# Kernel optimization log

Measured on AMD Instinct MI355X. Metric: run time of the kernel, lower is better.

## Reference

```python
import jax, jax.numpy as jnp
import numpy as np

TEMPERATURE = 0.5
EPS = 1e-8  # torch.nn.CosineSimilarity default eps


def setup_inputs() -> dict:
    key = jax.random.key(0)
    k1, k2 = jax.random.split(key)
    B, D = 4096, 256
    z1 = jax.random.normal(k1, (B, D), dtype=jnp.float32)
    # z2 = perturbed view of z1 so positive cosine sims are positive
    # (original torch code takes log of the RAW cosine sim, which is NaN
    #  for negative positives; realistic SimCLR positives are correlated views)
    z2 = z1 + 0.1 * jax.random.normal(k2, (B, D), dtype=jnp.float32)
    return {"z1": z1, "z2": z2}


def reference(z1, z2):
    B = z1.shape[0]
    z = jnp.concatenate([z1, z2], axis=0)                      # [2B, D]
    norm = jnp.maximum(jnp.linalg.norm(z, axis=-1, keepdims=True), EPS)
    zn = z / norm
    sim = zn @ zn.T                                            # [2B, 2B] cosine sims
    # positives: sim[i, i+B] and sim[i+B, i] (RAW cosine, per original code)
    pos = jnp.concatenate([jnp.diagonal(sim, offset=B),
                           jnp.diagonal(sim, offset=-B)])      # [2B]
    # mask self-similarity diagonal to -inf before exp-sum
    diag = jnp.eye(2 * B, dtype=bool)
    sim_masked = jnp.where(diag, -jnp.inf, sim)
    denom = jnp.sum(jnp.exp(sim_masked / TEMPERATURE), axis=-1)  # [2B]
    loss = -jnp.mean(jnp.log(pos / denom))
    return loss
```

## Files before the change

### kernel.cpp

```cpp
#include <hip/hip_runtime.h>
#include <hip/hip_bf16.h>


#define NROWS 8192
#define BHALF 4096
#define DDIM  256

typedef __attribute__((ext_vector_type(4))) int   i32x4;
typedef __attribute__((ext_vector_type(8))) int   i32x8;
typedef __attribute__((ext_vector_type(4))) float f32x4;

#define SCALE1 0x7F7F7F7F
#define TWO_LOG2E 2.8853900817779268f

__device__ __forceinline__ void load_lds16(const unsigned char* g, unsigned char* l) {
    __builtin_amdgcn_global_load_lds(
        (const __attribute__((address_space(1))) void*)g,
        (__attribute__((address_space(3))) void*)l, 16, 0, 0);
}

__global__ __launch_bounds__(256) void prep_kernel(const float* __restrict__ z1,
                                                   const float* __restrict__ z2,
                                                   unsigned char* __restrict__ zn8,
                                                   float* __restrict__ posPart,
                                                   float* __restrict__ out) {
    __shared__ float sp[4];
    int wave = threadIdx.x >> 6;
    int lane = threadIdx.x & 63;
    int i    = blockIdx.x * 4 + wave;
    float4 a = reinterpret_cast<const float4*>(z1 + (size_t)i * DDIM)[lane];
    float4 b = reinterpret_cast<const float4*>(z2 + (size_t)i * DDIM)[lane];
    float ss1 = a.x * a.x + a.y * a.y + a.z * a.z + a.w * a.w;
    float ss2 = b.x * b.x + b.y * b.y + b.z * b.z + b.w * b.w;
    float dd  = a.x * b.x + a.y * b.y + a.z * b.z + a.w * b.w;
    #pragma unroll
    for (int off = 32; off; off >>= 1) {
        ss1 += __shfl_xor(ss1, off);
        ss2 += __shfl_xor(ss2, off);
        dd  += __shfl_xor(dd, off);
    }
    float n1 = fmaxf(sqrtf(ss1), 1e-8f);
    float n2 = fmaxf(sqrtf(ss2), 1e-8f);
    float i1 = 1.0f / n1, i2 = 1.0f / n2;
    int pa = __builtin_amdgcn_cvt_pk_fp8_f32(a.x * i1, a.y * i1, 0, 0);
    pa     = __builtin_amdgcn_cvt_pk_fp8_f32(a.z * i1, a.w * i1, pa, 1);
    int pb = __builtin_amdgcn_cvt_pk_fp8_f32(b.x * i2, b.y * i2, 0, 0);
    pb     = __builtin_amdgcn_cvt_pk_fp8_f32(b.z * i2, b.w * i2, pb, 1);
    reinterpret_cast<int*>(zn8 + (size_t)i * DDIM)[lane] = pa;
    reinterpret_cast<int*>(zn8 + (size_t)(i + BHALF) * DDIM)[lane] = pb;
    if (lane == 0) sp[wave] = __logf(dd * i1 * i2);
    if (blockIdx.x == 0 && threadIdx.x == 64) out[0] = 0.0f;
    __syncthreads();
    if (threadIdx.x == 0)
        posPart[blockIdx.x] = sp[0] + sp[1] + sp[2] + sp[3];
}

__global__ __launch_bounds__(256, 3) void denom_kernel(const unsigned char* __restrict__ zn8,
                                                       float* __restrict__ P) {
    __shared__ __align__(16) unsigned char sMem[48 * 1024];
    unsigned char* sA  = sMem;
    unsigned char* sB0 = sMem + 32768;
    unsigned char* sB1 = sMem;
    float* red    = (float*)(sMem + 16384);
    float* colRed = red + 256;

    int x = blockIdx.x, y = blockIdx.y;
    int bi, bj;
    if (x > y) { bi = y;      bj = x - 1;  }
    else       { bi = 63 - y; bj = 63 - x; }
    int iBase = bi * 128;
    int jBase = bj * 128;
    bool isDiag = (bi == bj);

    int t    = threadIdx.x;
    int lane = t & 63;
    int wave = t >> 6;
    int col  = lane & 15;
    int quad = lane >> 4;
    int wm = wave >> 1, wn = wave & 1;

    int rowL  = t >> 4;
    int chunk = (t & 15) ^ rowL;

    {
        const unsigned char* gA = zn8 + (size_t)(iBase + rowL) * DDIM + chunk * 16;
        #pragma unroll
        for (int q = 0; q < 8; q++)
            load_lds16(gA + q * 4096, sA + t * 16 + q * 4096);
        const unsigned char* gB = zn8 + (size_t)(jBase + rowL) * DDIM + chunk * 16;
        #pragma unroll
        for (int q = 0; q < 4; q++)
            load_lds16(gB + q * 4096, sB0 + t * 16 + q * 4096);
    }
    __syncthreads();

    i32x8 af[4][2];
    {
        const unsigned char* aRow = sA + (size_t)(wm * 64 + col) * DDIM;
        #pragma unroll
        for (int mt = 0; mt < 4; mt++)
            #pragma unroll
            for (int ks = 0; ks < 2; ks++) {
                int g0 = ks * 8 + quad * 2;
                i32x4 lo = *(const i32x4*)(aRow + mt * 16 * DDIM + ((g0    ) ^ col) * 16);
                i32x4 hi = *(const i32x4*)(aRow + mt * 16 * DDIM + ((g0 + 1) ^ col) * 16);
                af[mt][ks] = __builtin_shufflevector(lo, hi, 0, 1, 2, 3, 4, 5, 6, 7);
            }
    }
    __syncthreads();

    {
        const unsigned char* gB = zn8 + (size_t)(jBase + 64 + rowL) * DDIM + chunk * 16;
        #pragma unroll
        for (int q = 0; q < 4; q++)
            load_lds16(gB + q * 4096, sB1 + t * 16 + q * 4096);
    }

    float rs[4][4];
    #pragma unroll
    for (int mt = 0; mt < 4; mt++)
        #pragma unroll
        for (int r = 0; r < 4; r++) rs[mt][r] = 0.f;

    #pragma unroll
    for (int h = 0; h < 2; h++) {
        if (h) __syncthreads();
        const unsigned char* bRow =
            (h ? sB1 : sB0) + (size_t)(wn * 32 + col) * DDIM;

        i32x8 bfr[2][2];
        #pragma unroll
        for (int nt = 0; nt < 2; nt++)
            #pragma unroll
            for (int ks = 0; ks < 2; ks++) {
                int g0 = ks * 8 + quad * 2;
                i32x4 lo = *(const i32x4*)(bRow + nt * 16 * DDIM + ((g0    ) ^ col) * 16);
                i32x4 hi = *(const i32x4*)(bRow + nt * 16 * DDIM + ((g0 + 1) ^ col) * 16);
                bfr[nt][ks] = __builtin_shufflevector(lo, hi, 0, 1, 2, 3, 4, 5, 6, 7);
            }

        float cs[2] = {0.f, 0.f};
        #pragma unroll
        for (int mt = 0; mt < 4; mt++) {
            int gi = iBase + wm * 64 + mt * 16;
            #pragma unroll
            for (int nt = 0; nt < 2; nt++) {
                f32x4 acc = {0.f, 0.f, 0.f, 0.f};
                acc = __builtin_amdgcn_mfma_scale_f32_16x16x128_f8f6f4(
                          af[mt][0], bfr[nt][0], acc, 0, 0, 0, SCALE1, 0, SCALE1);
                acc = __builtin_amdgcn_mfma_scale_f32_16x16x128_f8f6f4(
                          af[mt][1], bfr[nt][1], acc, 0, 0, 0, SCALE1, 0, SCALE1);
                bool dtile = (gi == jBase + h * 64 + wn * 32 + nt * 16);
                float csl = 0.f;
                #pragma unroll
                for (int r = 0; r < 4; r++) {
                    float e = exp2f(acc[r] * TWO_LOG2E);
                    if (dtile && (quad * 4 + r) == col) e = 0.f;
                    rs[mt][r] += e;
                    csl += e;
                }
                cs[nt] += csl;
            }
        }

        if (!isDiag) {
            #pragma unroll
            for (int nt = 0; nt < 2; nt++) {
                float v = cs[nt];
                v += __shfl_xor(v, 16);
                v += __shfl_xor(v, 32);
                if (quad == 0)
                    colRed[wm * 128 + h * 64 + wn * 32 + nt * 16 + col] = v;
            }
        }
    }

    #pragma unroll
    for (int mt = 0; mt < 4; mt++)
        #pragma unroll
        for (int r = 0; r < 4; r++) {
            float v = rs[mt][r];
            v += __shfl_xor(v, 1);
            v += __shfl_xor(v, 2);
            v += __shfl_xor(v, 4);
            v += __shfl_xor(v, 8);
            rs[mt][r] = v;
        }
    __syncthreads();
    if (col == 0) {
        #pragma unroll
        for (int mt = 0; mt < 4; mt++)
            #pragma unroll
            for (int r = 0; r < 4; r++)
                red[wn * 128 + wm * 64 + mt * 16 + quad * 4 + r] = rs[mt][r];
    }
    __syncthreads();
    if (t < 128) {
        float* Prow = P + (((size_t)bi * 64 + bj) << 7);
        Prow[t] = red[t] + red[128 + t];
        if (!isDiag) {
            float* Pcol = P + (((size_t)bj * 64 + bi) << 7);
            Pcol[t] = colRed[t] + colRed[128 + t];
        }
    }
}

__global__ __launch_bounds__(256) void loss_kernel(const float* __restrict__ posPart,
                                                   const float* __restrict__ P,
                                                   float* __restrict__ out) {
    __shared__ float sdata[4];
    int t = threadIdx.x;
    int i = blockIdx.x * 256 + t;
    int bi = i >> 7, r = i & 127;
    const float* p = P + ((size_t)bi << 13) + r;
    float d0 = 0.f, d1 = 0.f, d2 = 0.f, d3 = 0.f;
    #pragma unroll
    for (int k = 0; k < 64; k += 4) {
        d0 += p[(k + 0) << 7];
        d1 += p[(k + 1) << 7];
        d2 += p[(k + 2) << 7];
        d3 += p[(k + 3) << 7];
    }
    float s = __logf((d0 + d1) + (d2 + d3));
    if (t < 32) s -= 2.0f * posPart[blockIdx.x * 32 + t];
    #pragma unroll
    for (int off = 32; off; off >>= 1) s += __shfl_xor(s, off);
    if ((t & 63) == 0) sdata[t >> 6] = s;
    __syncthreads();
    if (t == 0)
        atomicAdd(out, (sdata[0] + sdata[1] + sdata[2] + sdata[3]) * (1.0f / NROWS));
}

extern "C" void kernel_launch(void* const* d_in, const int* in_sizes, int n_in,
                              void* d_out, int out_size, void* d_ws, size_t ws_size,
                              hipStream_t stream) {
    const float* z1 = (const float*)d_in[0];
    const float* z2 = (const float*)d_in[1];

    unsigned char* zn8 = (unsigned char*)d_ws;
    float* P       = (float*)((char*)d_ws + (size_t)NROWS * DDIM);
    float* posPart = P + 64 * 64 * 128;

    prep_kernel<<<BHALF / 4, 256, 0, stream>>>(z1, z2, zn8, posPart, (float*)d_out);
    denom_kernel<<<dim3(65, 32), 256, 0, stream>>>(zn8, P);
    loss_kernel<<<NROWS / 256, 256, 0, stream>>>(posPart, P, (float*)d_out);
}
```

Measured before the change: 86.59 us.

## Process four column tiles per block with triple-buffered LDS pipeline

Each denom block now keeps its A row-tile in registers and sweeps up to four consecutive upper-triangular column tiles, streaming B half-tiles through a three-buffer LDS ring with explicit vmcnt waits so loads overlap MFMA/exp work. This cuts the grid from 2080 blocks to 544 and amortises the A load across tiles. Per-wave partial sums are written directly to a doubled P buffer instead of going through LDS reductions, and loss_kernel reads twice as many partials to match. The fixed buffer rotation and per-row tile distribution add complexity and can leave some blocks doing redundant clamped work on the last tile. With fewer blocks there is also less parallelism across CUs.

Result: slower. 105.9 us (+22.3%).

```diff
diff --git a/kernel.cpp b/kernel.cpp
--- a/kernel.cpp
+++ b/kernel.cpp
@@ -58,19 +58,15 @@
 __global__ __launch_bounds__(256, 3) void denom_kernel(const unsigned char* __restrict__ zn8,
                                                        float* __restrict__ P) {
     __shared__ __align__(16) unsigned char sMem[48 * 1024];
-    unsigned char* sA  = sMem;
-    unsigned char* sB0 = sMem + 32768;
-    unsigned char* sB1 = sMem;
-    float* red    = (float*)(sMem + 16384);
-    float* colRed = red + 256;
-
-    int x = blockIdx.x, y = blockIdx.y;
-    int bi, bj;
-    if (x > y) { bi = y;      bj = x - 1;  }
-    else       { bi = 63 - y; bj = 63 - x; }
+    unsigned char* buf0 = sMem;
+    unsigned char* buf1 = sMem + 16384;
+    unsigned char* buf2 = sMem + 32768;
+
+    int b = blockIdx.x;
+    int bi = 0;
+    while (true) { int c = (67 - bi) >> 2; if (b < c) break; b -= c; bi++; }
+    int bjStart = bi + b * 4;
     int iBase = bi * 128;
-    int jBase = bj * 128;
-    bool isDiag = (bi == bj);
 
     int t    = threadIdx.x;
     int lane = t & 63;
@@ -82,21 +78,25 @@
     int rowL  = t >> 4;
     int chunk = (t & 15) ^ rowL;
 
-    {
-        const unsigned char* gA = zn8 + (size_t)(iBase + rowL) * DDIM + chunk * 16;
-        #pragma unroll
-        for (int q = 0; q < 8; q++)
-            load_lds16(gA + q * 4096, sA + t * 16 + q * 4096);
-        const unsigned char* gB = zn8 + (size_t)(jBase + rowL) * DDIM + chunk * 16;
-        #pragma unroll
-        for (int q = 0; q < 4; q++)
-            load_lds16(gB + q * 4096, sB0 + t * 16 + q * 4096);
-    }
-    __syncthreads();
+    unsigned char* bufs[3] = { buf0, buf1, buf2 };
+
+    #define STAGE_HALF(R, DST)                                                  \
+        {                                                                       \
+            const unsigned char* _g = zn8 + (size_t)((R) + rowL) * DDIM + chunk * 16; \
+            _Pragma("unroll")                                                   \
+            for (int q = 0; q < 4; q++)                                         \
+                load_lds16(_g + q * 4096, (DST) + t * 16 + q * 4096);           \
+        }
+
+    STAGE_HALF(iBase,          buf0);
+    STAGE_HALF(iBase + 64,     buf1);
+    STAGE_HALF(bjStart * 128,  buf2);
+    asm volatile("s_waitcnt vmcnt(4)" ::: "memory");
+    __builtin_amdgcn_s_barrier();
 
     i32x8 af[4][2];
     {
-        const unsigned char* aRow = sA + (size_t)(wm * 64 + col) * DDIM;
+        const unsigned char* aRow = (wm ? buf1 : buf0) + (size_t)col * DDIM;
         #pragma unroll
         for (int mt = 0; mt < 4; mt++)
             #pragma unroll
@@ -107,26 +107,35 @@
                 af[mt][ks] = __builtin_shufflevector(lo, hi, 0, 1, 2, 3, 4, 5, 6, 7);
             }
     }
-    __syncthreads();
-
-    {
-        const unsigned char* gB = zn8 + (size_t)(jBase + 64 + rowL) * DDIM + chunk * 16;
-        #pragma unroll
-        for (int q = 0; q < 4; q++)
-            load_lds16(gB + q * 4096, sB1 + t * 16 + q * 4096);
-    }
+    asm volatile("s_waitcnt lgkmcnt(0)" ::: "memory");
+    __builtin_amdgcn_sched_barrier(0);
+    __builtin_amdgcn_s_barrier();
+
+    STAGE_HALF(bjStart * 128 + 64, buf0);
 
     float rs[4][4];
-    #pragma unroll
-    for (int mt = 0; mt < 4; mt++)
-        #pragma unroll
-        for (int r = 0; r < 4; r++) rs[mt][r] = 0.f;
-
-    #pragma unroll
-    for (int h = 0; h < 2; h++) {
-        if (h) __syncthreads();
-        const unsigned char* bRow =
-            (h ? sB1 : sB0) + (size_t)(wn * 32 + col) * DDIM;
+
+    #pragma unroll
+    for (int k = 0; k < 8; k++) {
+        const int tt = k >> 1, hh = k & 1;
+        int bjv      = bjStart + tt;
+        bool valid   = (bjv <= 63);
+        int bj       = valid ? bjv : 63;
+        int jBase    = bj * 128;
+        bool isDiag  = (bi == bj);
+
+        {
+            int s    = (k + 2 > 7) ? 7 : (k + 2);
+            int tts  = s >> 1;
+            int bjs_ = bjStart + tts;
+            int bjs  = (bjs_ <= 63) ? bjs_ : 63;
+            STAGE_HALF(bjs * 128 + (s & 1) * 64, bufs[(2 + s) % 3]);
+        }
+
+        asm volatile("s_waitcnt vmcnt(8)" ::: "memory");
+        __builtin_amdgcn_s_barrier();
+
+        const unsigned char* bRow = bufs[(2 + k) % 3] + (size_t)(wn * 32 + col) * DDIM;
 
         i32x8 bfr[2][2];
         #pragma unroll
@@ -138,6 +147,13 @@
                 i32x4 hi = *(const i32x4*)(bRow + nt * 16 * DDIM + ((g0 + 1) ^ col) * 16);
                 bfr[nt][ks] = __builtin_shufflevector(lo, hi, 0, 1, 2, 3, 4, 5, 6, 7);
             }
+
+        if (hh == 0) {
+            #pragma unroll
+            for (int mt = 0; mt < 4; mt++)
+                #pragma unroll
+                for (int r = 0; r < 4; r++) rs[mt][r] = 0.f;
+        }
 
         float cs[2] = {0.f, 0.f};
         #pragma unroll
@@ -150,7 +166,7 @@
                           af[mt][0], bfr[nt][0], acc, 0, 0, 0, SCALE1, 0, SCALE1);
                 acc = __builtin_amdgcn_mfma_scale_f32_16x16x128_f8f6f4(
                           af[mt][1], bfr[nt][1], acc, 0, 0, 0, SCALE1, 0, SCALE1);
-                bool dtile = (gi == jBase + h * 64 + wn * 32 + nt * 16);
+                bool dtile = (gi == jBase + hh * 64 + wn * 32 + nt * 16);
                 float csl = 0.f;
                 #pragma unroll
                 for (int r = 0; r < 4; r++) {
@@ -163,46 +179,41 @@
             }
         }
 
-        if (!isDiag) {
+        if (valid && !isDiag) {
             #pragma unroll
             for (int nt = 0; nt < 2; nt++) {
                 float v = cs[nt];
                 v += __shfl_xor(v, 16);
                 v += __shfl_xor(v, 32);
                 if (quad == 0)
-                    colRed[wm * 128 + h * 64 + wn * 32 + nt * 16 + col] = v;
-            }
-        }
-    }
-
-    #pragma unroll
-    for (int mt = 0; mt < 4; mt++)
-        #pragma unroll
-        for (int r = 0; r < 4; r++) {
-            float v = rs[mt][r];
-            v += __shfl_xor(v, 1);
-            v += __shfl_xor(v, 2);
-            v += __shfl_xor(v, 4);
-            v += __shfl_xor(v, 8);
-            rs[mt][r] = v;
-        }
-    __syncthreads();
-    if (col == 0) {
-        #pragma unroll
-        for (int mt = 0; mt < 4; mt++)
-            #pragma unroll
-            for (int r = 0; r < 4; r++)
-                red[wn * 128 + wm * 64 + mt * 16 + quad * 4 + r] = rs[mt][r];
-    }
-    __syncthreads();
-    if (t < 128) {
-        float* Prow = P + (((size_t)bi * 64 + bj) << 7);
-        Prow[t] = red[t] + red[128 + t];
-        if (!isDiag) {
-            float* Pcol = P + (((size_t)bj * 64 + bi) << 7);
-            Pcol[t] = colRed[t] + colRed[128 + t];
-        }
-    }
+                    P[(((size_t)bj * 64 + bi) * 2 + wm) * 128
+                      + hh * 64 + wn * 32 + nt * 16 + col] = v;
+            }
+        }
+
+        if (hh == 1) {
+            #pragma unroll
+            for (int mt = 0; mt < 4; mt++)
+                #pragma unroll
+                for (int r = 0; r < 4; r++) {
+                    float v = rs[mt][r];
+                    v += __shfl_xor(v, 1);
+                    v += __shfl_xor(v, 2);
+                    v += __shfl_xor(v, 4);
+                    v += __shfl_xor(v, 8);
+                    rs[mt][r] = v;
+                }
+            if (valid && col == 0) {
+                float* Pr = P + (((size_t)bi * 64 + bj) * 2 + wn) * 128;
+                #pragma unroll
+                for (int mt = 0; mt < 4; mt++) {
+                    f32x4 v4 = { rs[mt][0], rs[mt][1], rs[mt][2], rs[mt][3] };
+                    *reinterpret_cast<f32x4*>(Pr + wm * 64 + mt * 16 + quad * 4) = v4;
+                }
+            }
+        }
+    }
+    #undef STAGE_HALF
 }
 
 __global__ __launch_bounds__(256) void loss_kernel(const float* __restrict__ posPart,
@@ -212,10 +223,10 @@
     int t = threadIdx.x;
     int i = blockIdx.x * 256 + t;
     int bi = i >> 7, r = i & 127;
-    const float* p = P + ((size_t)bi << 13) + r;
+    const float* p = P + ((size_t)bi << 14) + r;
     float d0 = 0.f, d1 = 0.f, d2 = 0.f, d3 = 0.f;
     #pragma unroll
-    for (int k = 0; k < 64; k += 4) {
+    for (int k = 0; k < 128; k += 4) {
         d0 += p[(k + 0) << 7];
         d1 += p[(k + 1) << 7];
         d2 += p[(k + 2) << 7];
@@ -239,9 +250,9 @@
 
     unsigned char* zn8 = (unsigned char*)d_ws;
     float* P       = (float*)((char*)d_ws + (size_t)NROWS * DDIM);
-    float* posPart = P + 64 * 64 * 128;
+    float* posPart = P + (size_t)64 * 64 * 2 * 128;
 
     prep_kernel<<<BHALF / 4, 256, 0, stream>>>(z1, z2, zn8, posPart, (float*)d_out);
-    denom_kernel<<<dim3(65, 32), 256, 0, stream>>>(zn8, P);
+    denom_kernel<<<544, 256, 0, stream>>>(zn8, P);
     loss_kernel<<<NROWS / 256, 256, 0, stream>>>(posPart, P, (float*)d_out);
 }
```

## Make each wave own a 64x64 tile, loading fragments straight from global

Applied to the files above, without the earlier changes.

The denominator kernel stops having a 256-thread block share a 128x128 tile staged through LDS. Each wave now handles its own 64x64 upper-triangular tile and loads its FP8 MFMA fragments directly from global memory into registers, with no LDS and no __syncthreads. Row and column partial sums are written straight to a 128x128x64 partials array, and the loss kernel is adjusted to the new layout. This removes barrier and LDS staging overhead and improves load balance, but it adds more redundant global/L2 traffic per MAC and more partials for the loss kernel to read.

New measurement: 103.5 us. +19.5%, slower.

```diff
diff --git a/kernel.cpp b/kernel.cpp
--- a/kernel.cpp
+++ b/kernel.cpp
@@ -12,12 +12,6 @@
 
 #define SCALE1 0x7F7F7F7F
 #define TWO_LOG2E 2.8853900817779268f
-
-__device__ __forceinline__ void load_lds16(const unsigned char* g, unsigned char* l) {
-    __builtin_amdgcn_global_load_lds(
-        (const __attribute__((address_space(1))) void*)g,
-        (__attribute__((address_space(3))) void*)l, 16, 0, 0);
-}
 
 __global__ __launch_bounds__(256) void prep_kernel(const float* __restrict__ z1,
                                                    const float* __restrict__ z2,
@@ -55,122 +49,58 @@
         posPart[blockIdx.x] = sp[0] + sp[1] + sp[2] + sp[3];
 }
 
-__global__ __launch_bounds__(256, 3) void denom_kernel(const unsigned char* __restrict__ zn8,
-                                                       float* __restrict__ P) {
-    __shared__ __align__(16) unsigned char sMem[48 * 1024];
-    unsigned char* sA  = sMem;
-    unsigned char* sB0 = sMem + 32768;
-    unsigned char* sB1 = sMem;
-    float* red    = (float*)(sMem + 16384);
-    float* colRed = red + 256;
-
-    int x = blockIdx.x, y = blockIdx.y;
-    int bi, bj;
-    if (x > y) { bi = y;      bj = x - 1;  }
-    else       { bi = 63 - y; bj = 63 - x; }
-    int iBase = bi * 128;
-    int jBase = bj * 128;
-    bool isDiag = (bi == bj);
-
+__global__ __launch_bounds__(256) void denom_kernel(const unsigned char* __restrict__ zn8,
+                                                    float* __restrict__ P) {
     int t    = threadIdx.x;
     int lane = t & 63;
-    int wave = t >> 6;
     int col  = lane & 15;
     int quad = lane >> 4;
-    int wm = wave >> 1, wn = wave & 1;
 
-    int rowL  = t >> 4;
-    int chunk = (t & 15) ^ rowL;
+    int w = blockIdx.x * 4 + (t >> 6);
+    int y = w / 129, x = w - y * 129;
+    int ti, tj;
+    if (x > y) { ti = y;       tj = x - 1;   }
+    else       { ti = 127 - y; tj = 127 - x; }
+    int iBase = ti * 64, jBase = tj * 64;
+    bool isDiag = (ti == tj);
 
-    {
-        const unsigned char* gA = zn8 + (size_t)(iBase + rowL) * DDIM + chunk * 16;
+    const unsigned char* aBase = zn8 + (size_t)(iBase + col) * DDIM + quad * 32;
+    const unsigned char* bBase = zn8 + (size_t)(jBase + col) * DDIM + quad * 32;
+
+    i32x8 af[4][2], bf[4][2];
+    #pragma unroll
+    for (int mt = 0; mt < 4; mt++)
         #pragma unroll
-        for (int q = 0; q < 8; q++)
-            load_lds16(gA + q * 4096, sA + t * 16 + q * 4096);
-        const unsigned char* gB = zn8 + (size_t)(jBase + rowL) * DDIM + chunk * 16;
-        #pragma unroll
-        for (int q = 0; q < 4; q++)
-            load_lds16(gB + q * 4096, sB0 + t * 16 + q * 4096);
-    }
-    __syncthreads();
-
-    i32x8 af[4][2];
-    {
-        const unsigned char* aRow = sA + (size_t)(wm * 64 + col) * DDIM;
-        #pragma unroll
-        for (int mt = 0; mt < 4; mt++)
-            #pragma unroll
-            for (int ks = 0; ks < 2; ks++) {
-                int g0 = ks * 8 + quad * 2;
-                i32x4 lo = *(const i32x4*)(aRow + mt * 16 * DDIM + ((g0    ) ^ col) * 16);
-                i32x4 hi = *(const i32x4*)(aRow + mt * 16 * DDIM + ((g0 + 1) ^ col) * 16);
-                af[mt][ks] = __builtin_shufflevector(lo, hi, 0, 1, 2, 3, 4, 5, 6, 7);
-            }
-    }
-    __syncthreads();
-
-    {
-        const unsigned char* gB = zn8 + (size_t)(jBase + 64 + rowL) * DDIM + chunk * 16;
-        #pragma unroll
-        for (int q = 0; q < 4; q++)
-            load_lds16(gB + q * 4096, sB1 + t * 16 + q * 4096);
-    }
+        for (int ks = 0; ks < 2; ks++) {
+            af[mt][ks] = *(const i32x8*)(aBase + mt * 16 * DDIM + ks * 128);
+            bf[mt][ks] = *(const i32x8*)(bBase + mt * 16 * DDIM + ks * 128);
+        }
 
     float rs[4][4];
+    float cs[4];
     #pragma unroll
     for (int mt = 0; mt < 4; mt++)
         #pragma unroll
         for (int r = 0; r < 4; r++) rs[mt][r] = 0.f;
+    #pragma unroll
+    for (int nt = 0; nt < 4; nt++) cs[nt] = 0.f;
 
     #pragma unroll
-    for (int h = 0; h < 2; h++) {
-        if (h) __syncthreads();
-        const unsigned char* bRow =
-            (h ? sB1 : sB0) + (size_t)(wn * 32 + col) * DDIM;
-
-        i32x8 bfr[2][2];
+    for (int mt = 0; mt < 4; mt++) {
         #pragma unroll
-        for (int nt = 0; nt < 2; nt++)
+        for (int nt = 0; nt < 4; nt++) {
+            f32x4 acc = {0.f, 0.f, 0.f, 0.f};
+            acc = __builtin_amdgcn_mfma_scale_f32_16x16x128_f8f6f4(
+                      af[mt][0], bf[nt][0], acc, 0, 0, 0, SCALE1, 0, SCALE1);
+            acc = __builtin_amdgcn_mfma_scale_f32_16x16x128_f8f6f4(
+                      af[mt][1], bf[nt][1], acc, 0, 0, 0, SCALE1, 0, SCALE1);
+            bool dtile = isDiag && (mt == nt);
             #pragma unroll
-            for (int ks = 0; ks < 2; ks++) {
-                int g0 = ks * 8 + quad * 2;
-                i32x4 lo = *(const i32x4*)(bRow + nt * 16 * DDIM + ((g0    ) ^ col) * 16);
-                i32x4 hi = *(const i32x4*)(bRow + nt * 16 * DDIM + ((g0 + 1) ^ col) * 16);
-                bfr[nt][ks] = __builtin_shufflevector(lo, hi, 0, 1, 2, 3, 4, 5, 6, 7);
-            }
-
-        float cs[2] = {0.f, 0.f};
-        #pragma unroll
-        for (int mt = 0; mt < 4; mt++) {
-            int gi = iBase + wm * 64 + mt * 16;
-            #pragma unroll
-            for (int nt = 0; nt < 2; nt++) {
-                f32x4 acc = {0.f, 0.f, 0.f, 0.f};
-                acc = __builtin_amdgcn_mfma_scale_f32_16x16x128_f8f6f4(
-                          af[mt][0], bfr[nt][0], acc, 0, 0, 0, SCALE1, 0, SCALE1);
-                acc = __builtin_amdgcn_mfma_scale_f32_16x16x128_f8f6f4(
-                          af[mt][1], bfr[nt][1], acc, 0, 0, 0, SCALE1, 0, SCALE1);
-                bool dtile = (gi == jBase + h * 64 + wn * 32 + nt * 16);
-                float csl = 0.f;
-                #pragma unroll
-                for (int r = 0; r < 4; r++) {
-                    float e = exp2f(acc[r] * TWO_LOG2E);
-                    if (dtile && (quad * 4 + r) == col) e = 0.f;
-                    rs[mt][r] += e;
-                    csl += e;
-                }
-                cs[nt] += csl;
-            }
-        }
-
-        if (!isDiag) {
-            #pragma unroll
-            for (int nt = 0; nt < 2; nt++) {
-                float v = cs[nt];
-                v += __shfl_xor(v, 16);
-                v += __shfl_xor(v, 32);
-                if (quad == 0)
-                    colRed[wm * 128 + h * 64 + wn * 32 + nt * 16 + col] = v;
+            for (int r = 0; r < 4; r++) {
+                float e = exp2f(acc[r] * TWO_LOG2E);
+                if (dtile && (quad * 4 + r) == col) e = 0.f;
+                rs[mt][r] += e;
+                cs[nt]    += e;
             }
         }
     }
@@ -186,21 +116,24 @@
             v += __shfl_xor(v, 8);
             rs[mt][r] = v;
         }
-    __syncthreads();
     if (col == 0) {
+        float* Prow = P + ((size_t)ti * 128 + tj) * 64;
         #pragma unroll
-        for (int mt = 0; mt < 4; mt++)
-            #pragma unroll
-            for (int r = 0; r < 4; r++)
-                red[wn * 128 + wm * 64 + mt * 16 + quad * 4 + r] = rs[mt][r];
+        for (int mt = 0; mt < 4; mt++) {
+            f32x4 v4 = { rs[mt][0], rs[mt][1], rs[mt][2], rs[mt][3] };
+            *reinterpret_cast<f32x4*>(Prow + mt * 16 + quad * 4) = v4;
+        }
     }
-    __syncthreads();
-    if (t < 128) {
-        float* Prow = P + (((size_t)bi * 64 + bj) << 7);
-        Prow[t] = red[t] + red[128 + t];
-        if (!isDiag) {
-            float* Pcol = P + (((size_t)bj * 64 + bi) << 7);
-            Pcol[t] = colRed[t] + colRed[128 + t];
+
+    if (!isDiag) {
+        float* Pcol = P + ((size_t)tj * 128 + ti) * 64;
+        #pragma unroll
+        for (int nt = 0; nt < 4; nt++) {
+            float v = cs[nt];
+            v += __shfl_xor(v, 16);
+            v += __shfl_xor(v, 32);
+            if (quad == 0)
+                Pcol[nt * 16 + col] = v;
         }
     }
 }
@@ -211,15 +144,15 @@
     __shared__ float sdata[4];
     int t = threadIdx.x;
     int i = blockIdx.x * 256 + t;
-    int bi = i >> 7, r = i & 127;
+    int bi = i >> 6, r = i & 63;
     const float* p = P + ((size_t)bi << 13) + r;
     float d0 = 0.f, d1 = 0.f, d2 = 0.f, d3 = 0.f;
     #pragma unroll
-    for (int k = 0; k < 64; k += 4) {
-        d0 += p[(k + 0) << 7];
-        d1 += p[(k + 1) << 7];
-        d2 += p[(k + 2) << 7];
-        d3 += p[(k + 3) << 7];
+    for (int k = 0; k < 128; k += 4) {
+        d0 += p[(k + 0) << 6];
+        d1 += p[(k + 1) << 6];
+        d2 += p[(k + 2) << 6];
+        d3 += p[(k + 3) << 6];
     }
     float s = __logf((d0 + d1) + (d2 + d3));
     if (t < 32) s -= 2.0f * posPart[blockIdx.x * 32 + t];
@@ -239,9 +172,9 @@
 
     unsigned char* zn8 = (unsigned char*)d_ws;
     float* P       = (float*)((char*)d_ws + (size_t)NROWS * DDIM);
-    float* posPart = P + 64 * 64 * 128;
+    float* posPart = P + (size_t)128 * 128 * 64;
 
     prep_kernel<<<BHALF / 4, 256, 0, stream>>>(z1, z2, zn8, posPart, (float*)d_out);
-    denom_kernel<<<dim3(65, 32), 256, 0, stream>>>(zn8, P);
+    denom_kernel<<<2064, 256, 0, stream>>>(zn8, P);
     loss_kernel<<<NROWS / 256, 256, 0, stream>>>(posPart, P, (float*)d_out);
 }
```

## Load A fragments directly from global, shrink LDS, write partial sums without LDS reduction

Applied to the files above, without the earlier changes.

A-operand fragments are now read straight from global memory into registers rather than staged through LDS, which cuts LDS to 32KB and may allow more blocks per CU. The end-of-kernel LDS reduction and its barriers are removed: each wave writes its row and column partial sums directly to a P buffer that is twice as large, and loss_kernel sums twice as many partials. The cost is uncoalesced global reads for A and more global write traffic and workspace.

Result: slower. 93.47 us (+7.9%).

```diff
diff --git a/kernel.cpp b/kernel.cpp
--- a/kernel.cpp
+++ b/kernel.cpp
@@ -57,12 +57,9 @@
 
 __global__ __launch_bounds__(256, 3) void denom_kernel(const unsigned char* __restrict__ zn8,
                                                        float* __restrict__ P) {
-    __shared__ __align__(16) unsigned char sMem[48 * 1024];
-    unsigned char* sA  = sMem;
-    unsigned char* sB0 = sMem + 32768;
-    unsigned char* sB1 = sMem;
-    float* red    = (float*)(sMem + 16384);
-    float* colRed = red + 256;
+    __shared__ __align__(16) unsigned char sMem[32 * 1024];
+    unsigned char* buf0 = sMem;
+    unsigned char* buf1 = sMem + 16384;
 
     int x = blockIdx.x, y = blockIdx.y;
     int bi, bj;
@@ -83,37 +80,27 @@
     int chunk = (t & 15) ^ rowL;
 
     {
-        const unsigned char* gA = zn8 + (size_t)(iBase + rowL) * DDIM + chunk * 16;
-        #pragma unroll
-        for (int q = 0; q < 8; q++)
-            load_lds16(gA + q * 4096, sA + t * 16 + q * 4096);
         const unsigned char* gB = zn8 + (size_t)(jBase + rowL) * DDIM + chunk * 16;
         #pragma unroll
         for (int q = 0; q < 4; q++)
-            load_lds16(gB + q * 4096, sB0 + t * 16 + q * 4096);
-    }
-    __syncthreads();
-
+            load_lds16(gB + q * 4096, buf0 + t * 16 + q * 4096);
+    }
+
+    const unsigned char* aBase = zn8 + (size_t)(iBase + wm * 64 + col) * DDIM + quad * 32;
     i32x8 af[4][2];
-    {
-        const unsigned char* aRow = sA + (size_t)(wm * 64 + col) * DDIM;
-        #pragma unroll
-        for (int mt = 0; mt < 4; mt++)
-            #pragma unroll
-            for (int ks = 0; ks < 2; ks++) {
-                int g0 = ks * 8 + quad * 2;
-                i32x4 lo = *(const i32x4*)(aRow + mt * 16 * DDIM + ((g0    ) ^ col) * 16);
-                i32x4 hi = *(const i32x4*)(aRow + mt * 16 * DDIM + ((g0 + 1) ^ col) * 16);
-                af[mt][ks] = __builtin_shufflevector(lo, hi, 0, 1, 2, 3, 4, 5, 6, 7);
-            }
-    }
+    #pragma unroll
+    for (int mt = 0; mt < 4; mt++)
+        #pragma unroll
+        for (int ks = 0; ks < 2; ks++)
+            af[mt][ks] = *(const i32x8*)(aBase + mt * 16 * DDIM + ks * 128);
+    __builtin_amdgcn_sched_barrier(0);
     __syncthreads();
 
     {
         const unsigned char* gB = zn8 + (size_t)(jBase + 64 + rowL) * DDIM + chunk * 16;
         #pragma unroll
         for (int q = 0; q < 4; q++)
-            load_lds16(gB + q * 4096, sB1 + t * 16 + q * 4096);
+            load_lds16(gB + q * 4096, buf1 + t * 16 + q * 4096);
     }
 
     float rs[4][4];
@@ -126,51 +113,44 @@
     for (int h = 0; h < 2; h++) {
         if (h) __syncthreads();
         const unsigned char* bRow =
-            (h ? sB1 : sB0) + (size_t)(wn * 32 + col) * DDIM;
-
-        i32x8 bfr[2][2];
-        #pragma unroll
-        for (int nt = 0; nt < 2; nt++)
+            (h ? buf1 : buf0) + (size_t)(wn * 32 + col) * DDIM;
+
+        #pragma unroll
+        for (int nt = 0; nt < 2; nt++) {
+            i32x8 bfr[2];
             #pragma unroll
             for (int ks = 0; ks < 2; ks++) {
                 int g0 = ks * 8 + quad * 2;
                 i32x4 lo = *(const i32x4*)(bRow + nt * 16 * DDIM + ((g0    ) ^ col) * 16);
                 i32x4 hi = *(const i32x4*)(bRow + nt * 16 * DDIM + ((g0 + 1) ^ col) * 16);
-                bfr[nt][ks] = __builtin_shufflevector(lo, hi, 0, 1, 2, 3, 4, 5, 6, 7);
+                bfr[ks] = __builtin_shufflevector(lo, hi, 0, 1, 2, 3, 4, 5, 6, 7);
             }
 
-        float cs[2] = {0.f, 0.f};
-        #pragma unroll
-        for (int mt = 0; mt < 4; mt++) {
-            int gi = iBase + wm * 64 + mt * 16;
+            float csn = 0.f;
             #pragma unroll
-            for (int nt = 0; nt < 2; nt++) {
+            for (int mt = 0; mt < 4; mt++) {
+                int gi = iBase + wm * 64 + mt * 16;
                 f32x4 acc = {0.f, 0.f, 0.f, 0.f};
                 acc = __builtin_amdgcn_mfma_scale_f32_16x16x128_f8f6f4(
-                          af[mt][0], bfr[nt][0], acc, 0, 0, 0, SCALE1, 0, SCALE1);
+                          af[mt][0], bfr[0], acc, 0, 0, 0, SCALE1, 0, SCALE1);
                 acc = __builtin_amdgcn_mfma_scale_f32_16x16x128_f8f6f4(
-                          af[mt][1], bfr[nt][1], acc, 0, 0, 0, SCALE1, 0, SCALE1);
+                          af[mt][1], bfr[1], acc, 0, 0, 0, SCALE1, 0, SCALE1);
                 bool dtile = (gi == jBase + h * 64 + wn * 32 + nt * 16);
-                float csl = 0.f;
                 #pragma unroll
                 for (int r = 0; r < 4; r++) {
                     float e = exp2f(acc[r] * TWO_LOG2E);
                     if (dtile && (quad * 4 + r) == col) e = 0.f;
                     rs[mt][r] += e;
-                    csl += e;
+                    csn       += e;
                 }
-                cs[nt] += csl;
             }
-        }
-
-        if (!isDiag) {
-            #pragma unroll
-            for (int nt = 0; nt < 2; nt++) {
-                float v = cs[nt];
-                v += __shfl_xor(v, 16);
-                v += __shfl_xor(v, 32);
+
+            if (!isDiag) {
+                csn += __shfl_xor(csn, 16);
+                csn += __shfl_xor(csn, 32);
                 if (quad == 0)
-                    colRed[wm * 128 + h * 64 + wn * 32 + nt * 16 + col] = v;
+                    P[(((size_t)bj * 64 + bi) * 2 + wm) * 128
+                      + h * 64 + wn * 32 + nt * 16 + col] = csn;
             }
         }
     }
@@ -186,21 +166,12 @@
             v += __shfl_xor(v, 8);
             rs[mt][r] = v;
         }
-    __syncthreads();
     if (col == 0) {
-        #pragma unroll
-        for (int mt = 0; mt < 4; mt++)
-            #pragma unroll
-            for (int r = 0; r < 4; r++)
-                red[wn * 128 + wm * 64 + mt * 16 + quad * 4 + r] = rs[mt][r];
-    }
-    __syncthreads();
-    if (t < 128) {
-        float* Prow = P + (((size_t)bi * 64 + bj) << 7);
-        Prow[t] = red[t] + red[128 + t];
-        if (!isDiag) {
-            float* Pcol = P + (((size_t)bj * 64 + bi) << 7);
-            Pcol[t] = colRed[t] + colRed[128 + t];
+        float* Pr = P + (((size_t)bi * 64 + bj) * 2 + wn) * 128;
+        #pragma unroll
+        for (int mt = 0; mt < 4; mt++) {
+            f32x4 v4 = { rs[mt][0], rs[mt][1], rs[mt][2], rs[mt][3] };
+            *reinterpret_cast<f32x4*>(Pr + wm * 64 + mt * 16 + quad * 4) = v4;
         }
     }
 }
@@ -212,10 +183,10 @@
     int t = threadIdx.x;
     int i = blockIdx.x * 256 + t;
     int bi = i >> 7, r = i & 127;
-    const float* p = P + ((size_t)bi << 13) + r;
+    const float* p = P + ((size_t)bi << 14) + r;
     float d0 = 0.f, d1 = 0.f, d2 = 0.f, d3 = 0.f;
     #pragma unroll
-    for (int k = 0; k < 64; k += 4) {
+    for (int k = 0; k < 128; k += 4) {
         d0 += p[(k + 0) << 7];
         d1 += p[(k + 1) << 7];
         d2 += p[(k + 2) << 7];
@@ -239,7 +210,7 @@
 
     unsigned char* zn8 = (unsigned char*)d_ws;
     float* P       = (float*)((char*)d_ws + (size_t)NROWS * DDIM);
-    float* posPart = P + 64 * 64 * 128;
+    float* posPart = P + (size_t)64 * 64 * 2 * 128;
 
     prep_kernel<<<BHALF / 4, 256, 0, stream>>>(z1, z2, zn8, posPart, (float*)d_out);
     denom_kernel<<<dim3(65, 32), 256, 0, stream>>>(zn8, P);
```
